# Kernel optimization log

Measured on AMD Instinct MI355X. Metric: run time of the kernel, lower is better.

## Reference

```python
import jax, jax.numpy as jnp
import numpy as np
from jax import lax

EPS = 1e-5
B, NA, NE, NAL = 1024, 10, 10, 9

def qbn(x):
    # QBN_RM1d: divide by RMS of detached input over all dims but last
    xd = lax.stop_gradient(x)
    mean2 = jnp.mean((xd * xd).reshape(-1, xd.shape[-1]), axis=0)
    return x / jnpp_sqrt(mean2) if False else x / jnp.sqrt(mean2 + EPS)

def qrelu(x):
    # Qrelu1d: scale each 2-vector (axis -2) by mod/max(1,mod), mod from detached x
    xd = lax.stop_gradient(x)
    mod = jnp.sqrt(jnp.sum(xd * xd, axis=-2))
    coeff = mod / jnp.maximum(1.0, mod)
    return x * coeff[..., None, :]

def rcn(x, Ws):
    for W in Ws:
        x = qrelu(qbn(x @ W))
    return x

def qmerge(x):
    return jnp.sum(x * x, axis=-2)

def qmaxpool(x):
    # x: [B,A,N,2,C]; pick per-channel entity with max squared 2-norm
    xd = lax.stop_gradient(x)
    mod = jnp.sum(xd * xd, axis=-2)            # [B,A,N,C]
    idx = jnp.argmax(mod, axis=-2)             # [B,A,C]
    idxb = jnp.broadcast_to(idx[:, :, None, None, :], x.shape[:2] + (1,) + x.shape[-2:])
    return jnp.take_along_axis(x, idxb, axis=-3)[:, :, 0]   # [B,A,2,C]

def build_vec(feats, own_vec):
    # feats: [B,A,n,9]; own_vec: [B,A,2,11]
    pos = feats[..., 2:4][..., None]                          # [B,A,n,2,1]
    pos_mod = jnp.sqrt(jnp.sum(pos * pos, axis=-2))           # [B,A,n,1]
    other = jnp.concatenate([feats[..., :2], feats[..., 4:]], axis=-1)  # [B,A,n,7]
    other_mod = jnp.sqrt(2.0 * other * other)                 # repeat-2 then 2-norm = sqrt(2*x^2)
    mask = pos_mod == 0.0
    denom = jnp.where(mask, 1.0, pos_mod)
    coff = jnp.where(mask, 0.0, other_mod / denom)[..., None, :]   # [B,A,n,1,7]
    vec = pos * coff                                           # [B,A,n,2,7]
    own_mod = jnp.sqrt(jnp.sum(own_vec * own_vec, axis=-2))[:, :, None, :]  # [B,A,1,11]
    own_coff = jnp.where(mask, 0.0, own_mod / denom)[..., None, :]          # [B,A,n,1,11]
    own_vecf = pos * own_coff                                  # [B,A,n,2,11]
    return jnp.concatenate([pos, vec, own_vecf], axis=-1)      # [B,A,n,2,19]

def setup_inputs() -> dict:
    key = jax.random.key(0)
    ks = jax.random.split(key, 32)
    s = 0.1
    inp = {
        'own_feats':   jax.random.normal(ks[0], (B, NA, 11), jnp.float32),
        'enemy_feats': jax.random.normal(ks[1], (B, NA, NE, 9), jnp.float32),
        'ally_feats':  jax.random.normal(ks[2], (B, NA, NAL, 9), jnp.float32),
        'W_e1': jax.random.normal(ks[3], (19, 64), jnp.float32) * s,
        'W_e2': jax.random.normal(ks[4], (64, 64), jnp.float32) * s,
        'W_a1': jax.random.normal(ks[5], (19, 64), jnp.float32) * s,
        'W_a2': jax.random.normal(ks[6], (64, 64), jnp.float32) * s,
        'W_f1': jax.random.normal(ks[7], (64, 64), jnp.float32) * s,
        'W_f2': jax.random.normal(ks[8], (64, 64), jnp.float32) * s,
        'W_ie1': jax.random.normal(ks[9], (128, 64), jnp.float32) * s,
        'W_ie2': jax.random.normal(ks[10], (64, 64), jnp.float32) * s,
        'W_ie3': jax.random.normal(ks[11], (64, 1), jnp.float32) * s,
        'W_ia1': jax.random.normal(ks[12], (128, 64), jnp.float32) * s,
        'W_ia2': jax.random.normal(ks[13], (64, 64), jnp.float32) * s,
        'W_ia3': jax.random.normal(ks[14], (64, 1), jnp.float32) * s,
        'W_oa1': jax.random.normal(ks[15], (64, 64), jnp.float32) * s,
        'b_oa1': jnp.zeros((64,), jnp.float32),
        'W_oa2': jax.random.normal(ks[16], (64, 3), jnp.float32) * s,
        'b_oa2': jnp.zeros((3,), jnp.float32),
        'W_at1': jax.random.normal(ks[17], (128, 128), jnp.float32) * s,
        'b_at1': jnp.zeros((128,), jnp.float32),
        'W_at2': jax.random.normal(ks[18], (128, 64), jnp.float32) * s,
        'b_at2': jnp.zeros((64,), jnp.float32),
        'W_at3': jax.random.normal(ks[19], (64, 1), jnp.float32) * s,
        'b_at3': jnp.zeros((1,), jnp.float32),
    }
    return inp

def reference(own_feats, enemy_feats, ally_feats,
              W_e1, W_e2, W_a1, W_a2, W_f1, W_f2,
              W_ie1, W_ie2, W_ie3, W_ia1, W_ia2, W_ia3,
              W_oa1, b_oa1, W_oa2, b_oa2,
              W_at1, b_at1, W_at2, b_at2, W_at3, b_at3):
    Bc = own_feats.shape[0]
    own_vec = jnp.repeat(own_feats[:, :, None, :], 2, axis=2)        # [B,A,2,11]
    ev = build_vec(enemy_feats, own_vec)                              # [B,A,10,2,19]
    av = build_vec(ally_feats, own_vec)                               # [B,A,9,2,19]
    e_rc = rcn(ev, (W_e1, W_e2))                                      # [B,A,10,2,64]
    e_scalar = qmerge(e_rc)                                           # [B,A,10,64]
    a_rc = rcn(av, (W_a1, W_a2))                                      # [B,A,9,2,64]
    all_rc = jnp.concatenate([e_rc, a_rc], axis=-3)                   # [B,A,19,2,64]
    vf = rcn(qmaxpool(all_rc), (W_f1, W_f2))                          # [B,A,2,64]
    vrep = jnp.broadcast_to(vf[:, :, None], (Bc, NA, NE, 2, 64))
    cat = jnp.concatenate([vrep, e_rc], axis=-1)                      # [B,A,10,2,128]
    e_imp = rcn(cat, (W_ie1, W_ie2, W_ie3))                           # [B,A,10,2,1]
    a_imp = rcn(cat, (W_ia1, W_ia2, W_ia3))                           # (orig code also uses enemy feats here)
    move_vec = jnp.sum(jnp.concatenate([e_imp, a_imp], axis=-3), axis=-3)  # [B,A,2,1]
    sf = qmerge(vf)                                                   # [B,A,64]
    oaq = jax.nn.relu(sf @ W_oa1 + b_oa1) @ W_oa2 + b_oa2             # [B,A,3]
    mmq = oaq[:, :, 2:3]
    up = mmq + move_vec[:, :, 1, :]
    down = mmq - move_vec[:, :, 1, :]
    right = mmq + move_vec[:, :, 0, :]
    left = mmq - move_vec[:, :, 0, :]
    move_q = jnp.concatenate([up, down, right, left], axis=-1)        # [B,A,4]
    sfr = jnp.broadcast_to(sf[:, :, None, :], (Bc, NA, NE, 64))
    atf = jnp.concatenate([sfr, e_scalar], axis=-1)                   # [B,A,10,128]
    h = jax.nn.relu(atf @ W_at1 + b_at1)
    h = jax.nn.relu(h @ W_at2 + b_at2)
    aq = (h @ W_at3 + b_at3)[..., 0]                                  # [B,A,10]
    return jnp.concatenate([oaq[:, :, 0:2], move_q, aq], axis=-1)     # [B,A,16]
```

## Files before the change

kernel.cpp:

```cpp
#include <hip/hip_runtime.h>
#include <math.h>

#define BATCH 1024
#define NA 10
#define NEN 10
#define NALY 9
#define NAG (BATCH*NA)
#define NEE (NAG*NEN)
#define NAE (NAG*NALY)
#define EPSF 1e-5f

#define DOFF_SE1 0
#define DOFF_SE2 1024
#define DOFF_SA1 2048
#define DOFF_SA2 3072
#define DOFF_SF1 4096
#define DOFF_SF2 5120
#define DOFF_SIE1 6144
#define DOFF_SIE2 7168
#define DOFF_SIA1 8192
#define DOFF_SIA2 9216
#define DOFF_SIE3 10240
#define DOFF_SIA3 10368
#define NDOUBLES 16384

#define NBLK_BE (NEE/8)
#define NBLK_BA (NAE/8)
#define NBLK_PE64 (NEE/64)
#define NBLK_PA64 (NAE/64)

__device__ __forceinline__ double sum16vd(const double* __restrict__ S, int ch) {
    double s = 0.0;
#pragma unroll
    for (int r = 0; r < 16; ++r) s += S[r*64 + ch];
    return s;
}
__device__ __forceinline__ double sum16sd8(const double* __restrict__ S) {
    double s = 0.0;
#pragma unroll
    for (int r = 0; r < 16; ++r) s += S[r*8];
    return s;
}
__device__ __forceinline__ float qbn_s(const double* __restrict__ S, int ch, double invRows) {
    float m = (float)(sum16vd(S, ch)*invRows);
    return sqrtf(m + EPSF);
}
__device__ __forceinline__ void red_to_S(const double* red, double* S, int bid, int tid) {
    if (tid < 64) {
        double v = red[tid] + red[tid+64] + red[tid+128] + red[tid+192];
        atomicAdd(&S[(bid & 15)*64 + tid], v);
    }
}
__device__ __forceinline__ float pair_m2(float x0, float x1) {
    return __fadd_rn(__fmul_rn(x0,x0), __fmul_rn(x1,x1));
}
__device__ __forceinline__ float qcoef(float mod) {
    return fminf(mod, 1.0f);
}

__global__ __launch_bounds__(256) void k_build_both(
    const float* __restrict__ ef, const float* __restrict__ af,
    const float* __restrict__ own,
    const float* __restrict__ We1, const float* __restrict__ Wa1,
    float* __restrict__ XE, float* __restrict__ XA,
    double* __restrict__ SE1, double* __restrict__ SA1)
{
    bool isA = (blockIdx.x >= NBLK_BE);
    int blk = isA ? (blockIdx.x - NBLK_BE) : blockIdx.x;
    const float* feats = isA ? af : ef;
    const float* W1    = isA ? Wa1 : We1;
    float* X           = isA ? XA : XE;
    double* S1         = isA ? SA1 : SE1;
    int nEntPerAgent   = isA ? NALY : NEN;

    __shared__ float wlds[19*64];
    __shared__ float gpc[16][19];
    __shared__ double red[256];
    int tid = threadIdx.x;
    for (int i = tid; i < 19*64; i += 256) wlds[i] = W1[i];
    if (tid < 152) {
        int el = tid / 19, chg = tid % 19;
        int ent = blk*8 + el;
        const float* f = feats + (size_t)ent*9;
        int agent = ent / nEntPerAgent;
        float px = f[2], py = f[3];
        float pm = sqrtf(__fadd_rn(__fmul_rn(px,px), __fmul_rn(py,py)));
        float val;
        if (chg == 0) val = 1.f;
        else if (chg < 8) {
            int j = chg - 1;
            int fi = (j < 2) ? j : (j + 2);
            float o = f[fi];
            float om = sqrtf(__fmul_rn(__fmul_rn(2.0f,o),o));
            val = (pm == 0.f) ? 0.f : __fdiv_rn(om, pm);
        } else {
            float o = own[(size_t)agent*11 + (chg-8)];
            float t = __fmul_rn(o,o);
            float om = sqrtf(__fadd_rn(t,t));
            val = (pm == 0.f) ? 0.f : __fdiv_rn(om, pm);
        }
        gpc[el*2 + 0][chg] = __fmul_rn(px, val);
        gpc[el*2 + 1][chg] = __fmul_rn(py, val);
    }
    __syncthreads();
    int l = tid >> 7, c = (tid >> 6) & 1, ch = tid & 63;
    float wreg[19];
#pragma unroll
    for (int k = 0; k < 19; ++k) wreg[k] = wlds[k*64+ch];
    double lr = 0.0;
#pragma unroll
    for (int i = 0; i < 4; ++i) {
        int el = l + 2*i;
        int ent = blk*8 + el;
        int row = el*2 + c;
        float acc = 0.f;
#pragma unroll
        for (int k = 18; k >= 0; --k) {
            acc = fmaf(gpc[row][k], wreg[k], acc);
        }
        X[(size_t)ent*128 + c*64 + ch] = acc;
        lr += (double)acc * (double)acc;
    }
    red[tid] = lr;
    __syncthreads();
    red_to_S(red, S1, blk, tid);
}

__device__ __forceinline__ void pair_layer_body(
    float* __restrict__ X, const double* __restrict__ Sin, double* __restrict__ Sout,
    const float* __restrict__ W, double invRows, int blk)
{
    __shared__ float wlds[4096];
    __shared__ __align__(16) float ybuf[64][132];
    __shared__ float ss[64];
    double* dredw = (double*)&ybuf[0][0];
    int tid = threadIdx.x;
    for (int i = tid; i < 4096; i += 512) wlds[i] = W[i];
    if (tid < 64) ss[tid] = qbn_s(Sin, tid, invRows);
    __syncthreads();
    int rl = tid >> 4;
    int ch0 = (tid & 15) * 4;
#pragma unroll
    for (int h = 0; h < 2; ++h) {
        int r = rl + h*32;
        size_t row = (size_t)blk*64 + r;
        float4 xv0 = *(const float4*)&X[row*128 + ch0];
        float4 xv1 = *(const float4*)&X[row*128 + 64 + ch0];
        float xs0[4] = {xv0.x,xv0.y,xv0.z,xv0.w};
        float xs1[4] = {xv1.x,xv1.y,xv1.z,xv1.w};
        float y0[4], y1[4];
#pragma unroll
        for (int i = 0; i < 4; ++i) {
            float s = ss[ch0+i];
            float u0 = xs0[i]/s, u1 = xs1[i]/s;
            float mod = sqrtf(pair_m2(u0,u1));
            float cf = qcoef(mod);
            y0[i] = __fmul_rn(u0,cf);
            y1[i] = __fmul_rn(u1,cf);
        }
        *(float4*)&ybuf[r][2*ch0]     = make_float4(y0[0],y1[0],y0[1],y1[1]);
        *(float4*)&ybuf[r][2*ch0 + 4] = make_float4(y0[2],y1[2],y0[3],y1[3]);
    }
    __syncthreads();
    float a0[4] = {0.f,0.f,0.f,0.f};
    float a1[4] = {0.f,0.f,0.f,0.f};
    float c0[4] = {0.f,0.f,0.f,0.f};
    float c1[4] = {0.f,0.f,0.f,0.f};
#pragma unroll
    for (int k = 63; k >= 1; k -= 2) {
        float4 wk  = *(const float4*)&wlds[k*64 + ch0];
        float4 wk1 = *(const float4*)&wlds[(k-1)*64 + ch0];
        float4 ya  = *(const float4*)&ybuf[rl][2*k - 2];
        float4 yb  = *(const float4*)&ybuf[rl+32][2*k - 2];
        float wkv[4]  = {wk.x,wk.y,wk.z,wk.w};
        float wk1v[4] = {wk1.x,wk1.y,wk1.z,wk1.w};
#pragma unroll
        for (int i = 0; i < 4; ++i) {
            a0[i] = fmaf(ya.z, wkv[i], a0[i]);
            a1[i] = fmaf(ya.w, wkv[i], a1[i]);
        }
#pragma unroll
        for (int i = 0; i < 4; ++i) {
            a0[i] = fmaf(ya.x, wk1v[i], a0[i]);
            a1[i] = fmaf(ya.y, wk1v[i], a1[i]);
        }
#pragma unroll
        for (int i = 0; i < 4; ++i) {
            c0[i] = fmaf(yb.z, wkv[i], c0[i]);
            c1[i] = fmaf(yb.w, wkv[i], c1[i]);
        }
#pragma unroll
        for (int i = 0; i < 4; ++i) {
            c0[i] = fmaf(yb.x, wk1v[i], c0[i]);
            c1[i] = fmaf(yb.y, wk1v[i], c1[i]);
        }
    }
    size_t rowA = (size_t)blk*64 + rl;
    size_t rowB = rowA + 32;
    *(float4*)&X[rowA*128 + ch0]      = make_float4(a0[0],a0[1],a0[2],a0[3]);
    *(float4*)&X[rowA*128 + 64 + ch0] = make_float4(a1[0],a1[1],a1[2],a1[3]);
    *(float4*)&X[rowB*128 + ch0]      = make_float4(c0[0],c0[1],c0[2],c0[3]);
    *(float4*)&X[rowB*128 + 64 + ch0] = make_float4(c1[0],c1[1],c1[2],c1[3]);
    __syncthreads();
    {
        int wv = tid >> 6;
#pragma unroll
        for (int i = 0; i < 4; ++i) {
            double d = (double)a0[i]*a0[i] + (double)a1[i]*a1[i]
                     + (double)c0[i]*c0[i] + (double)c1[i]*c1[i];
            d += __shfl_xor(d, 16, 64);
            d += __shfl_xor(d, 32, 64);
            if ((tid & 48) == 0) dredw[wv*64 + ch0+i] = d;
        }
    }
    __syncthreads();
    if (tid < 64) {
        double v = 0.0;
#pragma unroll
        for (int w = 0; w < 8; ++w) v += dredw[w*64 + tid];
        atomicAdd(&Sout[(blk & 15)*64 + tid], v);
    }
}

__global__ __launch_bounds__(512) void k_pair_both(
    float* __restrict__ XE, const double* __restrict__ SE1, double* __restrict__ SE2,
    const float* __restrict__ We2, double invRe,
    float* __restrict__ XA, const double* __restrict__ SA1, double* __restrict__ SA2,
    const float* __restrict__ Wa2, double invRa)
{
    if (blockIdx.x < NBLK_PE64)
        pair_layer_body(XE, SE1, SE2, We2, invRe, blockIdx.x);
    else
        pair_layer_body(XA, SA1, SA2, Wa2, invRa, blockIdx.x - NBLK_PE64);
}

__global__ __launch_bounds__(512) void k_pair_layer(
    float* __restrict__ X, const double* __restrict__ Sin, double* __restrict__ Sout,
    const float* __restrict__ W, double invRows)
{
    pair_layer_body(X, Sin, Sout, W, invRows, blockIdx.x);
}

__global__ __launch_bounds__(256) void k_finalize_pair(
    float* __restrict__ X, const double* __restrict__ S2, double invRows,
    float* __restrict__ ESC)
{
    __shared__ float ss[64];
    if (threadIdx.x < 64) ss[threadIdx.x] = qbn_s(S2, threadIdx.x, invRows);
    int t = blockIdx.x*256 + threadIdx.x;
    int rl = t >> 4;
    int ch0 = (t & 15) * 4;
    size_t base    = (size_t)rl*64 + ch0;
    size_t partner = (size_t)(rl ^ 1)*64 + ch0;
    float4 xv  = *(const float4*)&X[base];
    float4 xov = *(const float4*)&X[partner];
    __syncthreads();
    float xs[4]  = {xv.x,xv.y,xv.z,xv.w};
    float xos[4] = {xov.x,xov.y,xov.z,xov.w};
    float r[4], esc[4];
    int c = rl & 1;
#pragma unroll
    for (int i = 0; i < 4; ++i) {
        float s = ss[ch0+i];
        float u  = xs[i]/s;
        float uo = xos[i]/s;
        float u0 = (c==0) ? u : uo, u1 = (c==0) ? uo : u;
        float mod = sqrtf(pair_m2(u0,u1));
        float cf = qcoef(mod);
        r[i] = __fmul_rn(u, cf);
        if (c == 0) {
            float y1v = __fmul_rn(uo, cf);
            esc[i] = pair_m2(r[i], y1v);
        }
    }
    *(float4*)&X[base] = make_float4(r[0],r[1],r[2],r[3]);
    if (c == 0) {
        int ent = rl >> 1;
        *(float4*)&ESC[(size_t)ent*64 + ch0] = make_float4(esc[0],esc[1],esc[2],esc[3]);
    }
}

__global__ __launch_bounds__(256) void k_pool_f1(
    const float* __restrict__ XE, const float* __restrict__ XAraw,
    const double* __restrict__ SA2, double invRa,
    const float* __restrict__ Wf1, float* __restrict__ F1, double* __restrict__ Sf1)
{
    __shared__ float wlds[4096];
    __shared__ float v[4][2][64];
    __shared__ float ssa[64];
    __shared__ double red[256];
    int tid = threadIdx.x;
    for (int i = tid; i < 4096; i += 256) wlds[i] = Wf1[i];
    if (tid < 64) ssa[tid] = qbn_s(SA2, tid, invRa);
    __syncthreads();
    int grp = tid>>6, ch = tid&63;
    int agent = blockIdx.x*4 + grp;
    float best = -1.f, v0 = 0.f, v1 = 0.f;
    for (int e = 0; e < NEN; ++e) {
        size_t b = (size_t)(agent*NEN+e)*128;
        float x0 = XE[b+ch], x1 = XE[b+64+ch];
        float m2 = pair_m2(x0,x1);
        if (m2 > best) { best = m2; v0 = x0; v1 = x1; }
    }
    float sa = ssa[ch];
    for (int l = 0; l < NALY; ++l) {
        size_t b = (size_t)(agent*NALY+l)*128;
        float r0 = XAraw[b+ch], r1 = XAraw[b+64+ch];
        float u0 = r0/sa, u1 = r1/sa;
        float modf = sqrtf(pair_m2(u0,u1));
        float cff = qcoef(modf);
        float x0 = __fmul_rn(u0,cff), x1 = __fmul_rn(u1,cff);
        float m2 = pair_m2(x0,x1);
        if (m2 > best) { best = m2; v0 = x0; v1 = x1; }
    }
    v[grp][0][ch] = v0; v[grp][1][ch] = v1;
    __syncthreads();
    float a0 = 0.f, a1 = 0.f;
#pragma unroll
    for (int k = 0; k < 64; ++k) {
        float w = wlds[k*64+ch];
        a0 = fmaf(v[grp][0][k], w, a0);
        a1 = fmaf(v[grp][1][k], w, a1);
    }
    F1[(size_t)agent*128+ch] = a0; F1[(size_t)agent*128+64+ch] = a1;
    red[tid] = (double)a0*a0 + (double)a1*a1;
    __syncthreads();
    red_to_S(red, Sf1, blockIdx.x, tid);
}

__global__ __launch_bounds__(256) void k_vf_vtop(
    float* __restrict__ F1, const double* __restrict__ Sf2,
    float* __restrict__ SFb,
    const float* __restrict__ Wie1, const float* __restrict__ Wia1,
    const float* __restrict__ Wat1, const float* __restrict__ bat1,
    float* __restrict__ VTie, float* __restrict__ VTia, double invRows)
{
    __shared__ float wie[4096];
    __shared__ float wia[4096];
    __shared__ float vf[4][2][64];
    __shared__ float sfv[4][64];
    int tid = threadIdx.x;
    for (int i = tid; i < 4096; i += 256) { wie[i] = Wie1[i]; wia[i] = Wia1[i]; }
    int grp = tid>>6, ch = tid&63;
    int agent = blockIdx.x*4 + grp;
    float x0 = F1[(size_t)agent*128+ch], x1 = F1[(size_t)agent*128+64+ch];
    float s = qbn_s(Sf2, ch, invRows);
    float u0 = x0/s, u1 = x1/s;
    float mod = sqrtf(pair_m2(u0,u1));
    float cf = qcoef(mod);
    float y0 = __fmul_rn(u0,cf), y1 = __fmul_rn(u1,cf);
    vf[grp][0][ch] = y0; vf[grp][1][ch] = y1;
    float sf = pair_m2(y0,y1);
    SFb[(size_t)agent*64+ch] = sf;
    sfv[grp][ch] = sf;
    __syncthreads();
    float a0=0.f,a1=0.f,b0=0.f,b1=0.f;
    float at0 = bat1[ch], at1 = bat1[64+ch];
#pragma unroll
    for (int k = 0; k < 64; ++k) {
        float f0 = vf[grp][0][k], f1 = vf[grp][1][k];
        a0 = fmaf(f0, wie[k*64+ch], a0); a1 = fmaf(f1, wie[k*64+ch], a1);
        b0 = fmaf(f0, wia[k*64+ch], b0); b1 = fmaf(f1, wia[k*64+ch], b1);
        float sv = sfv[grp][k];
        at0 = fmaf(sv, Wat1[k*128 + ch], at0);
        at1 = fmaf(sv, Wat1[k*128 + 64 + ch], at1);
    }
    VTie[(size_t)agent*128+ch] = a0; VTie[(size_t)agent*128+64+ch] = a1;
    VTia[(size_t)agent*128+ch] = b0; VTia[(size_t)agent*128+64+ch] = b1;
    F1[(size_t)agent*128+ch] = at0; F1[(size_t)agent*128+64+ch] = at1;
}

__global__ __launch_bounds__(512) void k_imp1_both(
    float* __restrict__ XE,
    const float* __restrict__ VTe, const float* __restrict__ VTa,
    const float* __restrict__ W1e, const float* __restrict__ W1a,
    float* __restrict__ XIe,
    double* __restrict__ S1e, double* __restrict__ S1a)
{
    __shared__ float wldsE[4096];
    __shared__ float wldsA[4096];
    __shared__ __align__(16) float xt[64][68];
    double* dredwE = (double*)&xt[0][0];
    double* dredwA = dredwE + 512;
    int tid = threadIdx.x;
    for (int i = tid; i < 4096; i += 512) { wldsE[i] = W1e[4096 + i]; wldsA[i] = W1a[4096 + i]; }
#pragma unroll
    for (int i = 0; i < 2; ++i) {
        int fidx = tid + i*512;
        int r = fidx >> 4;
        int kq = (fidx & 15) * 4;
        float4 t4 = *(const float4*)&XE[(size_t)blockIdx.x*4096 + (size_t)fidx*4];
        *(float4*)&xt[r][kq] = t4;
    }
    __syncthreads();
    int rl = tid >> 4;
    int ch0 = (tid & 15) * 4;
    int entA = blockIdx.x*32 + (rl >> 1);
    int entB = entA + 16;
    int c = rl & 1;
    int agentA = entA / NEN, agentB = entB / NEN;
    float4 vteA = *(const float4*)&VTe[(size_t)agentA*128 + c*64 + ch0];
    float4 vtaA = *(const float4*)&VTa[(size_t)agentA*128 + c*64 + ch0];
    float4 vteB = *(const float4*)&VTe[(size_t)agentB*128 + c*64 + ch0];
    float4 vtaB = *(const float4*)&VTa[(size_t)agentB*128 + c*64 + ch0];
    float accEA[4] = {vteA.x, vteA.y, vteA.z, vteA.w};
    float accAA[4] = {vtaA.x, vtaA.y, vtaA.z, vtaA.w};
    float accEB[4] = {vteB.x, vteB.y, vteB.z, vteB.w};
    float accAB[4] = {vtaB.x, vtaB.y, vtaB.z, vtaB.w};
#pragma unroll
    for (int k = 0; k < 64; k += 4) {
        float4 xa4 = *(const float4*)&xt[rl][k];
        float4 xb4 = *(const float4*)&xt[rl+32][k];
        float xa[4] = {xa4.x, xa4.y, xa4.z, xa4.w};
        float xb[4] = {xb4.x, xb4.y, xb4.z, xb4.w};
#pragma unroll
        for (int kk = 0; kk < 4; ++kk) {
            float4 we = *(const float4*)&wldsE[(k+kk)*64 + ch0];
            accEA[0] = fmaf(xa[kk], we.x, accEA[0]);
            accEA[1] = fmaf(xa[kk], we.y, accEA[1]);
            accEA[2] = fmaf(xa[kk], we.z, accEA[2]);
            accEA[3] = fmaf(xa[kk], we.w, accEA[3]);
            accEB[0] = fmaf(xb[kk], we.x, accEB[0]);
            accEB[1] = fmaf(xb[kk], we.y, accEB[1]);
            accEB[2] = fmaf(xb[kk], we.z, accEB[2]);
            accEB[3] = fmaf(xb[kk], we.w, accEB[3]);
            float4 wa = *(const float4*)&wldsA[(k+kk)*64 + ch0];
            accAA[0] = fmaf(xa[kk], wa.x, accAA[0]);
            accAA[1] = fmaf(xa[kk], wa.y, accAA[1]);
            accAA[2] = fmaf(xa[kk], wa.z, accAA[2]);
            accAA[3] = fmaf(xa[kk], wa.w, accAA[3]);
            accAB[0] = fmaf(xb[kk], wa.x, accAB[0]);
            accAB[1] = fmaf(xb[kk], wa.y, accAB[1]);
            accAB[2] = fmaf(xb[kk], wa.z, accAB[2]);
            accAB[3] = fmaf(xb[kk], wa.w, accAB[3]);
        }
    }
    *(float4*)&XIe[(size_t)entA*128 + c*64 + ch0] = make_float4(accEA[0],accEA[1],accEA[2],accEA[3]);
    *(float4*)&XIe[(size_t)entB*128 + c*64 + ch0] = make_float4(accEB[0],accEB[1],accEB[2],accEB[3]);
    *(float4*)&XE [(size_t)entA*128 + c*64 + ch0] = make_float4(accAA[0],accAA[1],accAA[2],accAA[3]);
    *(float4*)&XE [(size_t)entB*128 + c*64 + ch0] = make_float4(accAB[0],accAB[1],accAB[2],accAB[3]);
    __syncthreads();
    int wv = tid >> 6;
#pragma unroll
    for (int i = 0; i < 4; ++i) {
        double dE = (double)accEA[i]*accEA[i] + (double)accEB[i]*accEB[i];
        dE += __shfl_xor(dE, 16, 64);
        dE += __shfl_xor(dE, 32, 64);
        double dA = (double)accAA[i]*accAA[i] + (double)accAB[i]*accAB[i];
        dA += __shfl_xor(dA, 16, 64);
        dA += __shfl_xor(dA, 32, 64);
        if ((tid & 48) == 0) {
            dredwE[wv*64 + ch0+i] = dE;
            dredwA[wv*64 + ch0+i] = dA;
        }
    }
    __syncthreads();
    if (tid < 64) {
        double vE = 0.0, vA = 0.0;
#pragma unroll
        for (int w = 0; w < 8; ++w) { vE += dredwE[w*64 + tid]; vA += dredwA[w*64 + tid]; }
        atomicAdd(&S1e[(blockIdx.x & 15)*64 + tid], vE);
        atomicAdd(&S1a[(blockIdx.x & 15)*64 + tid], vA);
    }
}

__global__ __launch_bounds__(256) void k_imp3_both(
    const float* __restrict__ XIe, const float* __restrict__ XIa,
    const double* __restrict__ S2e, const double* __restrict__ S2a,
    const float* __restrict__ W3e, const float* __restrict__ W3a,
    float* __restrict__ Ze, float* __restrict__ Za,
    double* __restrict__ S3e, double* __restrict__ S3a, double invRows)
{
    bool isA = (blockIdx.x >= (NEE/16));
    int blk = isA ? (blockIdx.x - NEE/16) : blockIdx.x;
    const float* XI = isA ? XIa : XIe;
    const double* S2 = isA ? S2a : S2e;
    const float* W3 = isA ? W3a : W3e;
    float* Z = isA ? Za : Ze;
    double* S3 = isA ? S3a : S3e;

    __shared__ float ss[64];
    __shared__ double red4[4];
    int tid = threadIdx.x; int grp = tid>>6, ch = tid&63;
    if (tid < 64) ss[tid] = qbn_s(S2, tid, invRows);
    __syncthreads();
    float s = ss[ch];
    double w3 = (double)W3[ch];
    double lr3 = 0.0;
#pragma unroll
    for (int i = 0; i < 4; ++i) {
        int ent = blk*16 + grp + 4*i;
        float x0 = XI[(size_t)ent*128+ch], x1 = XI[(size_t)ent*128+64+ch];
        float u0 = x0/s, u1 = x1/s;
        float mod = sqrtf(pair_m2(u0,u1));
        float cf = qcoef(mod);
        double v0 = (double)__fmul_rn(u0,cf) * w3;
        double v1 = (double)__fmul_rn(u1,cf) * w3;
#pragma unroll
        for (int m = 1; m < 64; m <<= 1) { v0 += __shfl_xor(v0,m,64); v1 += __shfl_xor(v1,m,64); }
        if (ch == 0) {
            float z0 = (float)v0, z1 = (float)v1;
            Z[(size_t)ent*2] = z0; Z[(size_t)ent*2+1] = z1;
            lr3 += (double)z0*z0 + (double)z1*z1;
        }
    }
    if (ch == 0) red4[grp] = lr3;
    __syncthreads();
    if (tid == 0) atomicAdd(&S3[(blk & 15)*8], red4[0]+red4[1]+red4[2]+red4[3]);
}

__global__ __launch_bounds__(256) void k_final_small(
    const float* __restrict__ Zie, const float* __restrict__ Zia,
    const double* __restrict__ Sie3, const double* __restrict__ Sia3,
    const float* __restrict__ SFb,
    const float* __restrict__ Woa1, const float* __restrict__ boa1,
    const float* __restrict__ Woa2, const float* __restrict__ boa2,
    float* __restrict__ out, double invRows)
{
    __shared__ float sflds[4][64];
    int tid = threadIdx.x; int grp = tid>>6, ch = tid&63;
    int agent = blockIdx.x*4 + grp;
    float sie = sqrtf((float)(sum16sd8(Sie3)*invRows) + EPSF);
    float sia = sqrtf((float)(sum16sd8(Sia3)*invRows) + EPSF);
    double pv0 = 0.0, pv1 = 0.0;
    if (ch < NEN) {
        int ent = agent*NEN + ch;
        float z0 = Zie[(size_t)ent*2]/sie, z1 = Zie[(size_t)ent*2+1]/sie;
        float mod = sqrtf(pair_m2(z0,z1)); float cf = qcoef(mod);
        pv0 = (double)__fmul_rn(z0,cf); pv1 = (double)__fmul_rn(z1,cf);
        z0 = Zia[(size_t)ent*2]/sia; z1 = Zia[(size_t)ent*2+1]/sia;
        mod = sqrtf(pair_m2(z0,z1)); cf = qcoef(mod);
        pv0 += (double)__fmul_rn(z0,cf); pv1 += (double)__fmul_rn(z1,cf);
    }
#pragma unroll
    for (int m = 1; m < 64; m <<= 1) { pv0 += __shfl_xor(pv0,m,64); pv1 += __shfl_xor(pv1,m,64); }
    sflds[grp][ch] = SFb[(size_t)agent*64+ch];
    __syncthreads();
    double hd = (double)boa1[ch];
#pragma unroll
    for (int k = 0; k < 64; ++k) hd += (double)sflds[grp][k]*(double)Woa1[k*64+ch];
    float h = fmaxf((float)hd, 0.f);
    double q0 = (double)h*(double)Woa2[ch*3+0];
    double q1 = (double)h*(double)Woa2[ch*3+1];
    double q2 = (double)h*(double)Woa2[ch*3+2];
#pragma unroll
    for (int m = 1; m < 64; m <<= 1) { q0 += __shfl_xor(q0,m,64); q1 += __shfl_xor(q1,m,64); q2 += __shfl_xor(q2,m,64); }
    if (ch == 0) {
        float oaq0 = (float)(q0 + (double)boa2[0]);
        float oaq1 = (float)(q1 + (double)boa2[1]);
        float mmq  = (float)(q2 + (double)boa2[2]);
        float mv0 = (float)pv0, mv1 = (float)pv1;
        float* o = out + (size_t)agent*16;
        o[0] = oaq0; o[1] = oaq1;
        o[2] = mmq + mv1; o[3] = mmq - mv1;
        o[4] = mmq + mv0; o[5] = mmq - mv0;
    }
}

__global__ __launch_bounds__(256) void k_attn(
    const float* __restrict__ ATtop, const float* __restrict__ ESC,
    const float* __restrict__ W1,
    const float* __restrict__ W2, const float* __restrict__ b2,
    const float* __restrict__ W3, const float* __restrict__ b3,
    float* __restrict__ out)
{
    __shared__ __align__(16) float escT[64][36];
    __shared__ __align__(16) float h1T[128][36];
    float (*h2)[68] = (float(*)[68])&escT[0][0];
    int tid = threadIdx.x;
    int row0 = blockIdx.x*32;
#pragma unroll
    for (int i = 0; i < 8; ++i) {
        int idx = tid + i*256; int r = idx>>6; int j = idx&63;
        escT[j][r] = ESC[(size_t)(row0 + r)*64 + j];
    }
    __syncthreads();
    {
        int j = tid & 127, rr = tid >> 7;
        float acc[16];
#pragma unroll
        for (int r = 0; r < 16; ++r) {
            int ent = row0 + rr*16 + r; int agent = ent/NEN;
            acc[r] = ATtop[(size_t)agent*128 + j];
        }
#pragma unroll 4
        for (int k = 0; k < 64; ++k) {
            float w = W1[(size_t)(64 + k)*128 + j];
            float4 a0 = *(const float4*)&escT[k][rr*16];
            float4 a1 = *(const float4*)&escT[k][rr*16 + 4];
            float4 a2 = *(const float4*)&escT[k][rr*16 + 8];
            float4 a3 = *(const float4*)&escT[k][rr*16 + 12];
            acc[0]  = fmaf(a0.x, w, acc[0]);
            acc[1]  = fmaf(a0.y, w, acc[1]);
            acc[2]  = fmaf(a0.z, w, acc[2]);
            acc[3]  = fmaf(a0.w, w, acc[3]);
            acc[4]  = fmaf(a1.x, w, acc[4]);
            acc[5]  = fmaf(a1.y, w, acc[5]);
            acc[6]  = fmaf(a1.z, w, acc[6]);
            acc[7]  = fmaf(a1.w, w, acc[7]);
            acc[8]  = fmaf(a2.x, w, acc[8]);
            acc[9]  = fmaf(a2.y, w, acc[9]);
            acc[10] = fmaf(a2.z, w, acc[10]);
            acc[11] = fmaf(a2.w, w, acc[11]);
            acc[12] = fmaf(a3.x, w, acc[12]);
            acc[13] = fmaf(a3.y, w, acc[13]);
            acc[14] = fmaf(a3.z, w, acc[14]);
            acc[15] = fmaf(a3.w, w, acc[15]);
        }
#pragma unroll
        for (int q = 0; q < 4; ++q) {
            float4 o = make_float4(fmaxf(acc[q*4+0],0.f), fmaxf(acc[q*4+1],0.f),
                                   fmaxf(acc[q*4+2],0.f), fmaxf(acc[q*4+3],0.f));
            *(float4*)&h1T[j][rr*16 + q*4] = o;
        }
    }
    __syncthreads();
    {
        int j2 = tid & 63, rr2 = tid >> 6;
        float bb = b2[j2];
        float acc[8];
#pragma unroll
        for (int r = 0; r < 8; ++r) acc[r] = bb;
#pragma unroll 8
        for (int k = 0; k < 128; ++k) {
            float w = W2[(size_t)k*64 + j2];
            float4 p0 = *(const float4*)&h1T[k][rr2*8];
            float4 p1 = *(const float4*)&h1T[k][rr2*8 + 4];
            acc[0] = fmaf(p0.x, w, acc[0]);
            acc[1] = fmaf(p0.y, w, acc[1]);
            acc[2] = fmaf(p0.z, w, acc[2]);
            acc[3] = fmaf(p0.w, w, acc[3]);
            acc[4] = fmaf(p1.x, w, acc[4]);
            acc[5] = fmaf(p1.y, w, acc[5]);
            acc[6] = fmaf(p1.z, w, acc[6]);
            acc[7] = fmaf(p1.w, w, acc[7]);
        }
#pragma unroll
        for (int r = 0; r < 8; ++r) h2[rr2*8+r][j2] = fmaxf(acc[r], 0.f);
    }
    __syncthreads();
    {
#pragma unroll
        for (int half = 0; half < 2; ++half) {
            int r3 = (tid >> 4) + half*16, l3 = tid & 15;
            float s = 0.f;
#pragma unroll
            for (int q = 0; q < 4; ++q) s = fmaf(h2[r3][l3 + 16*q], W3[l3 + 16*q], s);
#pragma unroll
            for (int m = 1; m < 16; m <<= 1) s += __shfl_xor(s, m, 64);
            if (l3 == 0) {
                int ent = row0 + r3; int agent = ent/NEN; int e = ent%NEN;
                out[(size_t)agent*16 + 6 + e] = s + b3[0];
            }
        }
    }
}

extern "C" void kernel_launch(void* const* d_in, const int* in_sizes, int n_in,
                              void* d_out, int out_size, void* d_ws, size_t ws_size,
                              hipStream_t stream) {
    const float* own  = (const float*)d_in[0];
    const float* ef   = (const float*)d_in[1];
    const float* af   = (const float*)d_in[2];
    const float* W_e1 = (const float*)d_in[3];
    const float* W_e2 = (const float*)d_in[4];
    const float* W_a1 = (const float*)d_in[5];
    const float* W_a2 = (const float*)d_in[6];
    const float* W_f1 = (const float*)d_in[7];
    const float* W_f2 = (const float*)d_in[8];
    const float* W_ie1= (const float*)d_in[9];
    const float* W_ie2= (const float*)d_in[10];
    const float* W_ie3= (const float*)d_in[11];
    const float* W_ia1= (const float*)d_in[12];
    const float* W_ia2= (const float*)d_in[13];
    const float* W_ia3= (const float*)d_in[14];
    const float* W_oa1= (const float*)d_in[15];
    const float* b_oa1= (const float*)d_in[16];
    const float* W_oa2= (const float*)d_in[17];
    const float* b_oa2= (const float*)d_in[18];
    const float* W_at1= (const float*)d_in[19];
    const float* b_at1= (const float*)d_in[20];
    const float* W_at2= (const float*)d_in[21];
    const float* b_at2= (const float*)d_in[22];
    const float* W_at3= (const float*)d_in[23];
    const float* b_at3= (const float*)d_in[24];
    float* out = (float*)d_out;
    float* wsf = (float*)d_ws;
    double* Sd = (double*)d_ws;

    size_t o = (size_t)NDOUBLES*2;
    float*  X_E  = wsf + o; o += (size_t)NEE*128;
    float*  X_A  = wsf + o; o += (size_t)NAE*128;
    float*  F1   = wsf + o; o += (size_t)NAG*128;
    float*  SFb  = wsf + o; o += (size_t)NAG*64;
    float*  VT_IE = wsf + o; o += (size_t)NAG*128;
    float*  VT_IA = wsf + o; o += (size_t)NAG*128;
    float*  XI   = wsf + o; o += (size_t)NEE*128;
    float*  Z_IE = wsf + o; o += (size_t)NEE*2;
    float*  Z_IA = wsf + o; o += (size_t)NEE*2;
    float*  ESC  = wsf + o; o += (size_t)NEE*64;

    double* S_E1 = Sd + DOFF_SE1;  double* S_E2 = Sd + DOFF_SE2;
    double* S_A1 = Sd + DOFF_SA1;  double* S_A2 = Sd + DOFF_SA2;
    double* S_F1 = Sd + DOFF_SF1;  double* S_F2 = Sd + DOFF_SF2;
    double* S_IE1= Sd + DOFF_SIE1; double* S_IE2= Sd + DOFF_SIE2;
    double* S_IA1= Sd + DOFF_SIA1; double* S_IA2= Sd + DOFF_SIA2;
    double* S_IE3= Sd + DOFF_SIE3; double* S_IA3= Sd + DOFF_SIA3;

    const double invRe = 1.0/(double)(NEE*2);
    const double invRa = 1.0/(double)(NAE*2);
    const double invRf = 1.0/(double)(NAG*2);

    hipMemsetAsync(Sd, 0, (size_t)NDOUBLES*sizeof(double), stream);

    k_build_both<<<NBLK_BE + NBLK_BA, 256, 0, stream>>>(
        ef, af, own, W_e1, W_a1, X_E, X_A, S_E1, S_A1);
    k_pair_both<<<NBLK_PE64 + NBLK_PA64, 512, 0, stream>>>(
        X_E, S_E1, S_E2, W_e2, invRe, X_A, S_A1, S_A2, W_a2, invRa);
    k_finalize_pair<<<NEE*32/256, 256, 0, stream>>>(X_E, S_E2, invRe, ESC);
    k_pool_f1<<<NAG/4, 256, 0, stream>>>(X_E, X_A, S_A2, invRa, W_f1, F1, S_F1);
    k_pair_layer<<<NAG/64, 512, 0, stream>>>(F1, S_F1, S_F2, W_f2, invRf);
    k_vf_vtop<<<NAG/4, 256, 0, stream>>>(F1, S_F2, SFb, W_ie1, W_ia1,
                                         W_at1, b_at1, VT_IE, VT_IA, invRf);
    k_imp1_both<<<NEE/32, 512, 0, stream>>>(X_E, VT_IE, VT_IA, W_ie1, W_ia1,
                                            XI, S_IE1, S_IA1);
    k_pair_both<<<NBLK_PE64 + NBLK_PE64, 512, 0, stream>>>(
        XI, S_IE1, S_IE2, W_ie2, invRe, X_E, S_IA1, S_IA2, W_ia2, invRe);
    k_imp3_both<<<2*(NEE/16), 256, 0, stream>>>(XI, X_E, S_IE2, S_IA2,
                                                W_ie3, W_ia3, Z_IE, Z_IA,
                                                S_IE3, S_IA3, invRe);

    k_final_small<<<NAG/4, 256, 0, stream>>>(Z_IE, Z_IA, S_IE3, S_IA3, SFb,
                                             W_oa1, b_oa1, W_oa2, b_oa2, out, invRe);
    k_attn<<<NEE/32, 256, 0, stream>>>(F1, ESC, W_at1, W_at2, b_at2,
                                       W_at3, b_at3, out);
}
```

Measured before the change: 534.8 us.

## Fold enemy pair finalization into pooling and imp1 kernels, dropping finalize pass

Result: no change. 536.4 us (median of 3 runs) (+0.3%).

```diff
diff --git a/kernel.cpp b/kernel.cpp
--- a/kernel.cpp
+++ b/kernel.cpp
@@ -241,64 +241,33 @@
     pair_layer_body(X, Sin, Sout, W, invRows, blockIdx.x);
 }
 
-__global__ __launch_bounds__(256) void k_finalize_pair(
-    float* __restrict__ X, const double* __restrict__ S2, double invRows,
-    float* __restrict__ ESC)
-{
-    __shared__ float ss[64];
-    if (threadIdx.x < 64) ss[threadIdx.x] = qbn_s(S2, threadIdx.x, invRows);
-    int t = blockIdx.x*256 + threadIdx.x;
-    int rl = t >> 4;
-    int ch0 = (t & 15) * 4;
-    size_t base    = (size_t)rl*64 + ch0;
-    size_t partner = (size_t)(rl ^ 1)*64 + ch0;
-    float4 xv  = *(const float4*)&X[base];
-    float4 xov = *(const float4*)&X[partner];
-    __syncthreads();
-    float xs[4]  = {xv.x,xv.y,xv.z,xv.w};
-    float xos[4] = {xov.x,xov.y,xov.z,xov.w};
-    float r[4], esc[4];
-    int c = rl & 1;
-#pragma unroll
-    for (int i = 0; i < 4; ++i) {
-        float s = ss[ch0+i];
-        float u  = xs[i]/s;
-        float uo = xos[i]/s;
-        float u0 = (c==0) ? u : uo, u1 = (c==0) ? uo : u;
-        float mod = sqrtf(pair_m2(u0,u1));
-        float cf = qcoef(mod);
-        r[i] = __fmul_rn(u, cf);
-        if (c == 0) {
-            float y1v = __fmul_rn(uo, cf);
-            esc[i] = pair_m2(r[i], y1v);
-        }
-    }
-    *(float4*)&X[base] = make_float4(r[0],r[1],r[2],r[3]);
-    if (c == 0) {
-        int ent = rl >> 1;
-        *(float4*)&ESC[(size_t)ent*64 + ch0] = make_float4(esc[0],esc[1],esc[2],esc[3]);
-    }
-}
-
 __global__ __launch_bounds__(256) void k_pool_f1(
-    const float* __restrict__ XE, const float* __restrict__ XAraw,
+    const float* __restrict__ XEraw, const float* __restrict__ XAraw,
+    const double* __restrict__ SE2, double invRe,
     const double* __restrict__ SA2, double invRa,
     const float* __restrict__ Wf1, float* __restrict__ F1, double* __restrict__ Sf1)
 {
     __shared__ float wlds[4096];
     __shared__ float v[4][2][64];
+    __shared__ float sse[64];
     __shared__ float ssa[64];
     __shared__ double red[256];
     int tid = threadIdx.x;
     for (int i = tid; i < 4096; i += 256) wlds[i] = Wf1[i];
-    if (tid < 64) ssa[tid] = qbn_s(SA2, tid, invRa);
+    if (tid < 64) { sse[tid] = qbn_s(SE2, tid, invRe); }
+    else if (tid < 128) { ssa[tid-64] = qbn_s(SA2, tid-64, invRa); }
     __syncthreads();
     int grp = tid>>6, ch = tid&63;
     int agent = blockIdx.x*4 + grp;
     float best = -1.f, v0 = 0.f, v1 = 0.f;
+    float se = sse[ch];
     for (int e = 0; e < NEN; ++e) {
         size_t b = (size_t)(agent*NEN+e)*128;
-        float x0 = XE[b+ch], x1 = XE[b+64+ch];
+        float r0 = XEraw[b+ch], r1 = XEraw[b+64+ch];
+        float u0 = r0/se, u1 = r1/se;
+        float modf = sqrtf(pair_m2(u0,u1));
+        float cff = qcoef(modf);
+        float x0 = __fmul_rn(u0,cff), x1 = __fmul_rn(u1,cff);
         float m2 = pair_m2(x0,x1);
         if (m2 > best) { best = m2; v0 = x0; v1 = x1; }
     }
@@ -372,18 +341,21 @@
 
 __global__ __launch_bounds__(512) void k_imp1_both(
     float* __restrict__ XE,
+    const double* __restrict__ SE2, double invRe,
     const float* __restrict__ VTe, const float* __restrict__ VTa,
     const float* __restrict__ W1e, const float* __restrict__ W1a,
-    float* __restrict__ XIe,
+    float* __restrict__ XIe, float* __restrict__ ESC,
     double* __restrict__ S1e, double* __restrict__ S1a)
 {
     __shared__ float wldsE[4096];
     __shared__ float wldsA[4096];
     __shared__ __align__(16) float xt[64][68];
+    __shared__ float sse[64];
     double* dredwE = (double*)&xt[0][0];
     double* dredwA = dredwE + 512;
     int tid = threadIdx.x;
     for (int i = tid; i < 4096; i += 512) { wldsE[i] = W1e[4096 + i]; wldsA[i] = W1a[4096 + i]; }
+    if (tid < 64) sse[tid] = qbn_s(SE2, tid, invRe);
 #pragma unroll
     for (int i = 0; i < 2; ++i) {
         int fidx = tid + i*512;
@@ -391,6 +363,30 @@
         int kq = (fidx & 15) * 4;
         float4 t4 = *(const float4*)&XE[(size_t)blockIdx.x*4096 + (size_t)fidx*4];
         *(float4*)&xt[r][kq] = t4;
+    }
+    __syncthreads();
+    {
+        int p = tid >> 4;
+        int ch0 = (tid & 15) * 4;
+        float4 x0v = *(const float4*)&xt[2*p][ch0];
+        float4 x1v = *(const float4*)&xt[2*p+1][ch0];
+        float xs0[4] = {x0v.x,x0v.y,x0v.z,x0v.w};
+        float xs1[4] = {x1v.x,x1v.y,x1v.z,x1v.w};
+        float y0[4], y1[4], esc[4];
+#pragma unroll
+        for (int i = 0; i < 4; ++i) {
+            float s = sse[ch0+i];
+            float u0 = xs0[i]/s, u1 = xs1[i]/s;
+            float mod = sqrtf(pair_m2(u0,u1));
+            float cf = qcoef(mod);
+            y0[i] = __fmul_rn(u0,cf);
+            y1[i] = __fmul_rn(u1,cf);
+            esc[i] = pair_m2(y0[i], y1[i]);
+        }
+        *(float4*)&xt[2*p][ch0]   = make_float4(y0[0],y0[1],y0[2],y0[3]);
+        *(float4*)&xt[2*p+1][ch0] = make_float4(y1[0],y1[1],y1[2],y1[3]);
+        int ent = blockIdx.x*32 + p;
+        *(float4*)&ESC[(size_t)ent*64 + ch0] = make_float4(esc[0],esc[1],esc[2],esc[3]);
     }
     __syncthreads();
     int rl = tid >> 4;
@@ -717,13 +713,13 @@
         ef, af, own, W_e1, W_a1, X_E, X_A, S_E1, S_A1);
     k_pair_both<<<NBLK_PE64 + NBLK_PA64, 512, 0, stream>>>(
         X_E, S_E1, S_E2, W_e2, invRe, X_A, S_A1, S_A2, W_a2, invRa);
-    k_finalize_pair<<<NEE*32/256, 256, 0, stream>>>(X_E, S_E2, invRe, ESC);
-    k_pool_f1<<<NAG/4, 256, 0, stream>>>(X_E, X_A, S_A2, invRa, W_f1, F1, S_F1);
+    k_pool_f1<<<NAG/4, 256, 0, stream>>>(X_E, X_A, S_E2, invRe, S_A2, invRa,
+                                         W_f1, F1, S_F1);
     k_pair_layer<<<NAG/64, 512, 0, stream>>>(F1, S_F1, S_F2, W_f2, invRf);
     k_vf_vtop<<<NAG/4, 256, 0, stream>>>(F1, S_F2, SFb, W_ie1, W_ia1,
                                          W_at1, b_at1, VT_IE, VT_IA, invRf);
-    k_imp1_both<<<NEE/32, 512, 0, stream>>>(X_E, VT_IE, VT_IA, W_ie1, W_ia1,
-                                            XI, S_IE1, S_IA1);
+    k_imp1_both<<<NEE/32, 512, 0, stream>>>(X_E, S_E2, invRe, VT_IE, VT_IA,
+                                            W_ie1, W_ia1, XI, ESC, S_IE1, S_IA1);
     k_pair_both<<<NBLK_PE64 + NBLK_PE64, 512, 0, stream>>>(
         XI, S_IE1, S_IE2, W_ie2, invRe, X_E, S_IA1, S_IA2, W_ia2, invRe);
     k_imp3_both<<<2*(NEE/16), 256, 0, stream>>>(XI, X_E, S_IE2, S_IA2,
```
